# Performance work log

Measured on AMD Instinct MI355X. Metric: run time of the kernel, lower is better.

## Reference

```python
import jax, jax.numpy as jnp
import numpy as np

G, KP, EPS = 4, 9, 1e-5  # deformable groups, 3x3 kernel points, BN eps


def setup_inputs() -> dict:
    key = jax.random.key(0)
    ks = jax.random.split(key, 16)
    N, C1, C2, H, W = 8, 256, 256, 64, 64
    c = int(C1 * 1.0) // 16 * 16  # 256 internal width
    OM = int(np.ceil(G * KP * 3 / 8) * 8)  # 112 padded offset/mask dim (108 used)
    sd = 0.02
    return {
        "x": jax.random.normal(ks[0], (N, C1, H, W), jnp.float32),
        "cv1_w": jax.random.normal(ks[1], (c, C1), jnp.float32) * sd,
        "cv1_b": jax.random.normal(ks[2], (c,), jnp.float32) * sd,
        "value_w": jax.random.normal(ks[3], (c, c), jnp.float32) * sd,
        "value_b": jax.random.normal(ks[4], (c,), jnp.float32) * sd,
        "dw_w": jax.random.normal(ks[5], (c,), jnp.float32) * sd + 1.0,
        "dw_b": jax.random.normal(ks[6], (c,), jnp.float32) * sd,
        "om_w": jax.random.normal(ks[7], (OM, c), jnp.float32) * sd,
        "om_b": jax.random.normal(ks[8], (OM,), jnp.float32) * sd,
        "out_w": jax.random.normal(ks[9], (c, c), jnp.float32) * sd,
        "cv2_w": jax.random.normal(ks[10], (C2, c), jnp.float32) * sd,
        "bn_gamma": jnp.ones((C2,), jnp.float32),
        "bn_beta": jnp.zeros((C2,), jnp.float32),
        "bn_mean": jax.random.normal(ks[11], (C2,), jnp.float32) * 0.1,
        "bn_var": jax.random.uniform(ks[12], (C2,), jnp.float32, minval=0.5, maxval=1.5),
    }


def _dcnv4(value, offset_mask, H, W):
    """DCNv4 core: offset-based bilinear sampling + unnormalized-mask aggregation.
    value: (N,H,W,c) NHWC features; offset_mask: (N,H,W,OM), per group layout
    [2*KP offsets (dx,dy pairs), KP masks]; no softmax on masks (DCNv4)."""
    N, c = value.shape[0], value.shape[-1]
    GC = c // G
    om = offset_mask[..., : G * KP * 3].reshape(N, H, W, G, 3 * KP)
    offs = om[..., : 2 * KP].reshape(N, H, W, G, KP, 2)  # (dx, dy), x = width axis
    mask = om[..., 2 * KP:]                               # (N,H,W,G,KP)
    ky, kx = jnp.meshgrid(jnp.arange(-1, 2, dtype=jnp.float32),
                          jnp.arange(-1, 2, dtype=jnp.float32), indexing="ij")
    kx, ky = kx.reshape(KP), ky.reshape(KP)               # 3x3 dilation-1 grid
    base_x = jnp.arange(W, dtype=jnp.float32)[None, None, :, None, None]
    base_y = jnp.arange(H, dtype=jnp.float32)[None, :, None, None, None]
    px = base_x + kx + offs[..., 0]                       # (N,H,W,G,KP) abs pixel x
    py = base_y + ky + offs[..., 1]
    x0, y0 = jnp.floor(px), jnp.floor(py)
    fx, fy = px - x0, py - y0
    x0i, y0i = x0.astype(jnp.int32), y0.astype(jnp.int32)
    vflat = value.reshape(N, H * W, G, GC).transpose(0, 2, 1, 3)  # (N,G,L,GC)
    acc = jnp.zeros((N, G, H, W, KP, GC), value.dtype)
    for dy, dx, wgt in ((0, 0, (1 - fy) * (1 - fx)), (0, 1, (1 - fy) * fx),
                        (1, 0, fy * (1 - fx)), (1, 1, fy * fx)):
        yy, xx = y0i + dy, x0i + dx
        valid = (yy >= 0) & (yy < H) & (xx >= 0) & (xx < W)   # zero padding
        idx = jnp.clip(yy, 0, H - 1) * W + jnp.clip(xx, 0, W - 1)
        idx_g = idx.transpose(0, 3, 1, 2, 4).reshape(N, G, H * W * KP)
        smp = jnp.take_along_axis(vflat, idx_g[..., None], axis=2)
        smp = smp.reshape(N, G, H, W, KP, GC)
        acc = acc + smp * (wgt * valid).transpose(0, 3, 1, 2, 4)[..., None]
    out = (acc * mask.transpose(0, 3, 1, 2, 4)[..., None]).sum(axis=4)  # (N,G,H,W,GC)
    return out.transpose(0, 2, 3, 1, 4).reshape(N, H, W, c)


def reference(x, cv1_w, cv1_b, value_w, value_b, dw_w, dw_b, om_w, om_b,
              out_w, cv2_w, bn_gamma, bn_beta, bn_mean, bn_var):
    N, C1, H, W = x.shape
    t = jnp.einsum("nchw,dc->nhwd", x, cv1_w) + cv1_b       # cv1 1x1 conv -> NHWC
    value = t @ value_w.T + value_b                          # DCNv4 value_proj
    om = (t * dw_w + dw_b) @ om_w.T + om_b                   # depthwise 1x1 + linear
    y = _dcnv4(value, om, H, W)
    y = y @ out_w.T                                          # output_proj (no bias)
    y = jnp.einsum("nhwc,dc->nhwd", y, cv2_w)                # cv2 1x1 (no bias)
    y = (y - bn_mean) * bn_gamma * jax.lax.rsqrt(bn_var + EPS) + bn_beta  # BN (eval)
    y = y * jax.nn.sigmoid(y)                                # SiLU
    return y.transpose(0, 3, 1, 2)                           # back to NCHW
```

## Files before the change

### kernel.cpp

```cpp
#include <hip/hip_runtime.h>
#include <hip/hip_bf16.h>
#include <math.h>

#define NN    8
#define HH    64
#define WW    64
#define HW    4096
#define NHW   32768
#define DALL  384
#define EPSBN 1e-5f

typedef __attribute__((ext_vector_type(8))) short short8v;
typedef __attribute__((ext_vector_type(4))) float f32x4;

__device__ __forceinline__ float b2f(unsigned short u) {
    union { unsigned int i; float f; } v; v.i = ((unsigned int)u) << 16; return v.f;
}
__device__ __forceinline__ unsigned short f2b(float f) {
    __hip_bfloat16 h = __float2bfloat16(f);
    return *reinterpret_cast<const unsigned short*>(&h);
}


__global__ __launch_bounds__(256)
void prep_kernel(const float* __restrict__ cv1_w, const float* __restrict__ cv1_b,
                 const float* __restrict__ value_w, const float* __restrict__ value_b,
                 const float* __restrict__ dw_w, const float* __restrict__ dw_b,
                 const float* __restrict__ om_w, const float* __restrict__ om_b,
                 const float* __restrict__ out_w, const float* __restrict__ cv2_w,
                 const float* __restrict__ bn_g, const float* __restrict__ bn_b,
                 const float* __restrict__ bn_m, const float* __restrict__ bn_v,
                 unsigned short* __restrict__ Wallbf, float* __restrict__ ball,
                 unsigned short* __restrict__ Woutbf, float* __restrict__ bout)
{
    int job = blockIdx.x * 256 + threadIdx.x;
    if (job < 65536) {
        int d = job >> 8, cc = job & 255;
        float s = 0.f;
        for (int e = 0; e < 256; ++e)
            s = fmaf(value_w[d*256+e], cv1_w[e*256+cc], s);
        Wallbf[job] = f2b(s);
    } else if (job < 94208) {
        int idx = job - 65536;
        int o = idx >> 8, cc = idx & 255;
        float s = 0.f;
        for (int e = 0; e < 256; ++e)
            s = fmaf(om_w[o*256+e]*dw_w[e], cv1_w[e*256+cc], s);
        Wallbf[job] = f2b(s);
    } else if (job < 98304) {
        Wallbf[job] = 0;
    } else if (job < 163840) {
        int idx = job - 98304;
        int d = idx >> 8;
        float s = 0.f;
        for (int e = 0; e < 256; ++e)
            s = fmaf(cv2_w[d*256+e], out_w[e*256 + (idx & 255)], s);
        float sc = bn_g[d] * rsqrtf(bn_v[d] + EPSBN);
        Woutbf[idx] = f2b(s * sc);
    } else if (job < 164096) {
        int d = job - 163840;
        float s = value_b[d];
        for (int e = 0; e < 256; ++e) s = fmaf(value_w[d*256+e], cv1_b[e], s);
        ball[d] = s;
    } else if (job < 164208) {
        int o = job - 164096;
        float s = om_b[o];
        for (int e = 0; e < 256; ++e)
            s = fmaf(om_w[o*256+e], fmaf(dw_w[e], cv1_b[e], dw_b[e]), s);
        ball[256 + o] = s;
    } else if (job < 164224) {
        ball[368 + job - 164208] = 0.f;
    } else if (job < 164480) {
        int d = job - 164224;
        float sc = bn_g[d] * rsqrtf(bn_v[d] + EPSBN);
        bout[d] = fmaf(-bn_m[d], sc, bn_b[d]);
    }
}

__global__ __launch_bounds__(256)
void cvt_tr_kernel(const float* __restrict__ x, unsigned short* __restrict__ xt)
{
    __shared__ float Ls[64][65];
    int p0 = blockIdx.x * 64;
    int c0 = blockIdx.y * 64;
    int n = p0 >> 12, hw0 = p0 & 4095;
    int t = threadIdx.x;
    #pragma unroll
    for (int i = 0; i < 16; ++i) {
        int idx = t + i * 256;
        int cc = idx >> 6, pp = idx & 63;
        Ls[cc][pp] = x[((size_t)(n*256 + c0 + cc))*4096 + hw0 + pp];
    }
    __syncthreads();
    #pragma unroll
    for (int i = 0; i < 8; ++i) {
        int idx = t + i * 256;
        int pp = idx >> 5, cp = idx & 31;
        int c = cp * 2;
        ushort2 v;
        v.x = f2b(Ls[c][pp]);
        v.y = f2b(Ls[c+1][pp]);
        *reinterpret_cast<ushort2*>(&xt[(size_t)(p0 + pp)*256 + c0 + c]) = v;
    }
}

__device__ __forceinline__
void gemm_mainloop(const unsigned short* __restrict__ A, const unsigned short* __restrict__ B,
                   int m0, int n0, unsigned short* As, unsigned short* Bs,
                   f32x4 (&acc)[4][4], int t)
{
    int lane = t & 63;
    int wv = t >> 6;
    int wr = wv >> 1, wc = wv & 1;
    int r_l = lane & 15;
    int kg_l = lane >> 4;

    for (int kt = 0; kt < 4; ++kt) {
        int c0 = kt * 64;
        #pragma unroll
        for (int i = 0; i < 4; ++i) {
            int idx = t + i * 256;
            int kg = idx & 7, row = idx >> 3;
            int soff = row*64 + ((kg ^ (row & 7)) << 3);
            *reinterpret_cast<short8v*>(&As[soff]) =
                *reinterpret_cast<const short8v*>(&A[(size_t)(m0 + row)*256 + c0 + kg*8]);
            *reinterpret_cast<short8v*>(&Bs[soff]) =
                *reinterpret_cast<const short8v*>(&B[(size_t)(n0 + row)*256 + c0 + kg*8]);
        }
        __syncthreads();
        #pragma unroll
        for (int ks = 0; ks < 2; ++ks) {
            short8v af[4], bfr[4];
            #pragma unroll
            for (int m = 0; m < 4; ++m) {
                int row = wr*64 + m*16 + r_l;
                af[m] = *reinterpret_cast<const short8v*>(
                    &As[row*64 + (((ks*4 + kg_l) ^ (row & 7)) << 3)]);
            }
            #pragma unroll
            for (int n = 0; n < 4; ++n) {
                int row = wc*64 + n*16 + r_l;
                bfr[n] = *reinterpret_cast<const short8v*>(
                    &Bs[row*64 + (((ks*4 + kg_l) ^ (row & 7)) << 3)]);
            }
            #pragma unroll
            for (int m = 0; m < 4; ++m)
                #pragma unroll
                for (int n = 0; n < 4; ++n)
                    acc[m][n] = __builtin_amdgcn_mfma_f32_16x16x32_bf16(af[m], bfr[n], acc[m][n], 0, 0, 0);
        }
        __syncthreads();
    }
}

__global__ __launch_bounds__(256)
void gemm_vo_kernel(const unsigned short* __restrict__ xt, const unsigned short* __restrict__ Wallbf,
                    const float* __restrict__ ball, unsigned short* __restrict__ VO)
{
    __shared__ unsigned short lds[2 * 8192];
    int t = threadIdx.x;
    int m0 = blockIdx.x * 128;
    int n0 = blockIdx.y * 128;
    f32x4 acc[4][4] = {};
    gemm_mainloop(xt, Wallbf, m0, n0, lds, lds + 8192, acc, t);

    int lane = t & 63;
    int wv = t >> 6, wr = wv >> 1, wc = wv & 1;
    int r_l = lane & 15, kg_l = lane >> 4;
    #pragma unroll
    for (int n = 0; n < 4; ++n) {
        int d = n0 + wc*64 + n*16 + r_l;
        float bb = ball[d];
        #pragma unroll
        for (int m = 0; m < 4; ++m) {
            int pr = m0 + wr*64 + m*16 + (kg_l << 2);
            #pragma unroll
            for (int r = 0; r < 4; ++r)
                VO[(size_t)(pr + r)*384 + d] = f2b(acc[m][n][r] + bb);
        }
    }
}

__global__ __launch_bounds__(256)
void gemm_out_kernel(const unsigned short* __restrict__ Woutbf, const unsigned short* __restrict__ y,
                     const float* __restrict__ bout, float* __restrict__ out)
{
    __shared__ unsigned short lds[2 * 8192];
    int t = threadIdx.x;
    int m0 = blockIdx.y * 128;
    int n0 = blockIdx.x * 128;
    f32x4 acc[4][4] = {};
    gemm_mainloop(Woutbf, y, m0, n0, lds, lds + 8192, acc, t);

    int lane = t & 63;
    int wv = t >> 6, wr = wv >> 1, wc = wv & 1;
    int r_l = lane & 15, kg_l = lane >> 4;
    int nimg = n0 >> 12;
    int hwb = n0 & 4095;
    #pragma unroll
    for (int m = 0; m < 4; ++m) {
        int dbase = m0 + wr*64 + m*16 + (kg_l << 2);
        #pragma unroll
        for (int r = 0; r < 4; ++r) {
            int d = dbase + r;
            float bb = bout[d];
            #pragma unroll
            for (int n = 0; n < 4; ++n) {
                int pcol = wc*64 + n*16 + r_l;
                float z = acc[m][n][r] + bb;
                float sv = z / (1.f + __expf(-z));
                out[((size_t)(nimg*256 + d))*4096 + hwb + pcol] = sv;
            }
        }
    }
}

__global__ __launch_bounds__(256)
void dcn_kernel(const unsigned short* __restrict__ VO, unsigned short* __restrict__ y)
{
    __shared__ float om_s[8][108];
    int t = threadIdx.x;
    int p0 = blockIdx.x * 8;

    for (int i = t; i < 864; i += 256) {
        int pl = i / 108, j = i - pl * 108;
        om_s[pl][j] = b2f(VO[(size_t)(p0 + pl)*384 + 256 + j]);
    }
    __syncthreads();

    int slot = t >> 3, ch8 = t & 7;
    int pl = slot >> 2, g = slot & 3;
    int p = p0 + pl;
    int hw = p & 4095;
    int h = hw >> 6, w = hw & 63;
    const unsigned short* vbase = VO + (size_t)(p >> 12) * (HW * (size_t)DALL) + g*64 + ch8*8;
    const float* o = &om_s[pl][g*27];

    float acc[8] = {};
    #pragma unroll
    for (int k = 0; k < 9; ++k) {
        float dxo = o[2*k], dyo = o[2*k+1], m = o[18+k];
        float pxf = (float)(w + (k % 3) - 1) + dxo;
        float pyf = (float)(h + (k / 3) - 1) + dyo;
        float x0f = floorf(pxf), y0f = floorf(pyf);
        float fx = pxf - x0f, fy = pyf - y0f;
        int x0 = (int)x0f, y0 = (int)y0f;
        #pragma unroll
        for (int dyy = 0; dyy < 2; ++dyy) {
            #pragma unroll
            for (int dxx = 0; dxx < 2; ++dxx) {
                int yy = y0 + dyy, xx = x0 + dxx;
                bool valid = (yy >= 0) & (yy < HH) & (xx >= 0) & (xx < WW);
                float wgt = (dyy ? fy : 1.f - fy) * (dxx ? fx : 1.f - fx);
                float wm = valid ? (m * wgt) : 0.f;
                int yc = min(max(yy, 0), HH - 1);
                int xc = min(max(xx, 0), WW - 1);
                short8v v = *reinterpret_cast<const short8v*>(
                    &vbase[(size_t)(yc * WW + xc) * DALL]);
                #pragma unroll
                for (int c = 0; c < 8; ++c)
                    acc[c] = fmaf(b2f((unsigned short)v[c]), wm, acc[c]);
            }
        }
    }
    short8v ov;
    #pragma unroll
    for (int c = 0; c < 8; ++c) ov[c] = (short)f2b(acc[c]);
    *reinterpret_cast<short8v*>(&y[(size_t)p*256 + g*64 + ch8*8]) = ov;
}

extern "C" void kernel_launch(void* const* d_in, const int* in_sizes, int n_in,
                              void* d_out, int out_size, void* d_ws, size_t ws_size,
                              hipStream_t stream) {
    const float* x       = (const float*)d_in[0];
    const float* cv1_w   = (const float*)d_in[1];
    const float* cv1_b   = (const float*)d_in[2];
    const float* value_w = (const float*)d_in[3];
    const float* value_b = (const float*)d_in[4];
    const float* dw_w    = (const float*)d_in[5];
    const float* dw_b    = (const float*)d_in[6];
    const float* om_w    = (const float*)d_in[7];
    const float* om_b    = (const float*)d_in[8];
    const float* out_w   = (const float*)d_in[9];
    const float* cv2_w   = (const float*)d_in[10];
    const float* bn_g    = (const float*)d_in[11];
    const float* bn_b    = (const float*)d_in[12];
    const float* bn_m    = (const float*)d_in[13];
    const float* bn_v    = (const float*)d_in[14];

    char* ws = (char*)d_ws;
    unsigned short* xt     = (unsigned short*)(ws);
    unsigned short* VO     = (unsigned short*)(ws + 16777216);
    unsigned short* y      = (unsigned short*)(ws + 41943040);
    unsigned short* Wallbf = (unsigned short*)(ws + 58720256);
    unsigned short* Woutbf = (unsigned short*)(ws + 58916864);
    float*          ball   = (float*)(ws + 59047936);
    float*          bout   = (float*)(ws + 59049472);
    float* out = (float*)d_out;

    prep_kernel<<<643, 256, 0, stream>>>(cv1_w, cv1_b, value_w, value_b, dw_w, dw_b,
                                         om_w, om_b, out_w, cv2_w,
                                         bn_g, bn_b, bn_m, bn_v,
                                         Wallbf, ball, Woutbf, bout);
    cvt_tr_kernel<<<dim3(512, 4), 256, 0, stream>>>(x, xt);
    gemm_vo_kernel<<<dim3(256, 3), 256, 0, stream>>>(xt, Wallbf, ball, VO);
    dcn_kernel<<<4096, 256, 0, stream>>>(VO, y);
    gemm_out_kernel<<<dim3(256, 2), 256, 0, stream>>>(Woutbf, y, bout, out);
}
```

Baseline: 95.96 us.

## Fuse NCHW transpose into value GEMM, tile DCN sampling via LDS, vectorize prep

Removes the separate fp32-to-bf16 transpose kernel: the value/offset GEMM now reads NCHW fp32 input directly, converts it in registers, and writes swizzled tiles into LDS. The DCN kernel now stages a 5x20 neighbourhood of value rows per 16-pixel chunk in shared memory and falls back to global loads only for out-of-tile samples. It also uses packed float2 FMAs. Prep loops get float4 loads with four independent accumulators. The costs are a larger LDS footprint, more blocks re-reading the 3x3 halo (each value tile is loaded by two group-half blocks), and a strided fp32 read pattern in the GEMM load.

```diff
diff --git a/kernel.cpp b/kernel.cpp
--- a/kernel.cpp
+++ b/kernel.cpp
@@ -12,6 +12,7 @@
 
 typedef __attribute__((ext_vector_type(8))) short short8v;
 typedef __attribute__((ext_vector_type(4))) float f32x4;
+typedef __attribute__((ext_vector_type(2))) float f32x2;
 
 __device__ __forceinline__ float b2f(unsigned short u) {
     union { unsigned int i; float f; } v; v.i = ((unsigned int)u) << 16; return v.f;
@@ -19,6 +20,12 @@
 __device__ __forceinline__ unsigned short f2b(float f) {
     __hip_bfloat16 h = __float2bfloat16(f);
     return *reinterpret_cast<const unsigned short*>(&h);
+}
+__device__ __forceinline__ f32x2 bf2x(int u) {
+    union { int i; float f; } a, b;
+    a.i = u << 16;
+    b.i = u & 0xffff0000;
+    f32x2 r; r[0] = a.f; r[1] = b.f; return r;
 }
 
 
@@ -36,27 +43,43 @@
     int job = blockIdx.x * 256 + threadIdx.x;
     if (job < 65536) {
         int d = job >> 8, cc = job & 255;
-        float s = 0.f;
-        for (int e = 0; e < 256; ++e)
-            s = fmaf(value_w[d*256+e], cv1_w[e*256+cc], s);
-        Wallbf[job] = f2b(s);
+        float s0=0.f, s1=0.f, s2=0.f, s3=0.f;
+        for (int e = 0; e < 256; e += 4) {
+            float4 wv = *reinterpret_cast<const float4*>(&value_w[d*256+e]);
+            s0 = fmaf(wv.x, cv1_w[(e+0)*256+cc], s0);
+            s1 = fmaf(wv.y, cv1_w[(e+1)*256+cc], s1);
+            s2 = fmaf(wv.z, cv1_w[(e+2)*256+cc], s2);
+            s3 = fmaf(wv.w, cv1_w[(e+3)*256+cc], s3);
+        }
+        Wallbf[job] = f2b((s0+s1)+(s2+s3));
     } else if (job < 94208) {
         int idx = job - 65536;
         int o = idx >> 8, cc = idx & 255;
-        float s = 0.f;
-        for (int e = 0; e < 256; ++e)
-            s = fmaf(om_w[o*256+e]*dw_w[e], cv1_w[e*256+cc], s);
-        Wallbf[job] = f2b(s);
+        float s0=0.f, s1=0.f, s2=0.f, s3=0.f;
+        for (int e = 0; e < 256; e += 4) {
+            float4 wv = *reinterpret_cast<const float4*>(&om_w[o*256+e]);
+            float4 dv = *reinterpret_cast<const float4*>(&dw_w[e]);
+            s0 = fmaf(wv.x*dv.x, cv1_w[(e+0)*256+cc], s0);
+            s1 = fmaf(wv.y*dv.y, cv1_w[(e+1)*256+cc], s1);
+            s2 = fmaf(wv.z*dv.z, cv1_w[(e+2)*256+cc], s2);
+            s3 = fmaf(wv.w*dv.w, cv1_w[(e+3)*256+cc], s3);
+        }
+        Wallbf[job] = f2b((s0+s1)+(s2+s3));
     } else if (job < 98304) {
         Wallbf[job] = 0;
     } else if (job < 163840) {
         int idx = job - 98304;
-        int d = idx >> 8;
-        float s = 0.f;
-        for (int e = 0; e < 256; ++e)
-            s = fmaf(cv2_w[d*256+e], out_w[e*256 + (idx & 255)], s);
+        int d = idx >> 8, cc = idx & 255;
+        float s0=0.f, s1=0.f, s2=0.f, s3=0.f;
+        for (int e = 0; e < 256; e += 4) {
+            float4 wv = *reinterpret_cast<const float4*>(&cv2_w[d*256+e]);
+            s0 = fmaf(wv.x, out_w[(e+0)*256+cc], s0);
+            s1 = fmaf(wv.y, out_w[(e+1)*256+cc], s1);
+            s2 = fmaf(wv.z, out_w[(e+2)*256+cc], s2);
+            s3 = fmaf(wv.w, out_w[(e+3)*256+cc], s3);
+        }
         float sc = bn_g[d] * rsqrtf(bn_v[d] + EPSBN);
-        Woutbf[idx] = f2b(s * sc);
+        Woutbf[idx] = f2b(((s0+s1)+(s2+s3)) * sc);
     } else if (job < 164096) {
         int d = job - 163840;
         float s = value_b[d];
@@ -78,29 +101,89 @@
 }
 
 __global__ __launch_bounds__(256)
-void cvt_tr_kernel(const float* __restrict__ x, unsigned short* __restrict__ xt)
+void gemm_vo_kernel(const float* __restrict__ x, const unsigned short* __restrict__ Wallbf,
+                    const float* __restrict__ ball, unsigned short* __restrict__ VO)
 {
-    __shared__ float Ls[64][65];
-    int p0 = blockIdx.x * 64;
-    int c0 = blockIdx.y * 64;
-    int n = p0 >> 12, hw0 = p0 & 4095;
+    __shared__ unsigned short As[8192];
+    __shared__ unsigned short Bs[8192];
     int t = threadIdx.x;
-    #pragma unroll
-    for (int i = 0; i < 16; ++i) {
-        int idx = t + i * 256;
-        int cc = idx >> 6, pp = idx & 63;
-        Ls[cc][pp] = x[((size_t)(n*256 + c0 + cc))*4096 + hw0 + pp];
-    }
-    __syncthreads();
-    #pragma unroll
-    for (int i = 0; i < 8; ++i) {
-        int idx = t + i * 256;
-        int pp = idx >> 5, cp = idx & 31;
-        int c = cp * 2;
-        ushort2 v;
-        v.x = f2b(Ls[c][pp]);
-        v.y = f2b(Ls[c+1][pp]);
-        *reinterpret_cast<ushort2*>(&xt[(size_t)(p0 + pp)*256 + c0 + c]) = v;
+    int m0 = blockIdx.x * 128;
+    int n0 = blockIdx.y * 128;
+    int nimg = m0 >> 12, hw0 = m0 & 4095;
+    int lane = t & 63;
+    int wv = t >> 6;
+    int wr = wv >> 1, wc = wv & 1;
+    int r_l = lane & 15, kg_l = lane >> 4;
+    int ci = t >> 6;
+    int l  = t & 63;
+
+    const float* xbase = x + (size_t)(nimg * 256) * 4096 + hw0;
+
+    f32x4 acc[4][4] = {};
+
+    for (int kt = 0; kt < 4; ++kt) {
+        int c0 = kt * 64;
+        float2 val[16];
+        #pragma unroll
+        for (int i = 0; i < 16; ++i)
+            val[i] = *reinterpret_cast<const float2*>(
+                &xbase[(size_t)(c0 + ci*16 + i) * 4096 + 2*l]);
+        __syncthreads();
+        #pragma unroll
+        for (int rsel = 0; rsel < 2; ++rsel) {
+            int row = 2*l + rsel;
+            #pragma unroll
+            for (int kgi = 0; kgi < 2; ++kgi) {
+                int kg = ci*2 + kgi;
+                short8v s;
+                #pragma unroll
+                for (int j = 0; j < 8; ++j)
+                    s[j] = (short)f2b(rsel ? val[kgi*8+j].y : val[kgi*8+j].x);
+                *reinterpret_cast<short8v*>(&As[row*64 + ((kg ^ (row & 7)) << 3)]) = s;
+            }
+        }
+        #pragma unroll
+        for (int i = 0; i < 4; ++i) {
+            int idx = t + i*256;
+            int row = idx >> 3, kg = idx & 7;
+            *reinterpret_cast<short8v*>(&Bs[row*64 + ((kg ^ (row & 7)) << 3)]) =
+                *reinterpret_cast<const short8v*>(&Wallbf[(size_t)(n0 + row)*256 + c0 + kg*8]);
+        }
+        __syncthreads();
+        #pragma unroll
+        for (int ks = 0; ks < 2; ++ks) {
+            short8v af[4], bfr[4];
+            #pragma unroll
+            for (int m = 0; m < 4; ++m) {
+                int row = wr*64 + m*16 + r_l;
+                af[m] = *reinterpret_cast<const short8v*>(
+                    &As[row*64 + (((ks*4 + kg_l) ^ (row & 7)) << 3)]);
+            }
+            #pragma unroll
+            for (int n = 0; n < 4; ++n) {
+                int row = wc*64 + n*16 + r_l;
+                bfr[n] = *reinterpret_cast<const short8v*>(
+                    &Bs[row*64 + (((ks*4 + kg_l) ^ (row & 7)) << 3)]);
+            }
+            #pragma unroll
+            for (int m = 0; m < 4; ++m)
+                #pragma unroll
+                for (int n = 0; n < 4; ++n)
+                    acc[m][n] = __builtin_amdgcn_mfma_f32_16x16x32_bf16(af[m], bfr[n], acc[m][n], 0, 0, 0);
+        }
+    }
+
+    #pragma unroll
+    for (int n = 0; n < 4; ++n) {
+        int d = n0 + wc*64 + n*16 + r_l;
+        float bb = ball[d];
+        #pragma unroll
+        for (int m = 0; m < 4; ++m) {
+            int pr = m0 + wr*64 + m*16 + (kg_l << 2);
+            #pragma unroll
+            for (int r = 0; r < 4; ++r)
+                VO[(size_t)(pr + r)*384 + d] = f2b(acc[m][n][r] + bb);
+        }
     }
 }
 
@@ -154,34 +237,6 @@
 }
 
 __global__ __launch_bounds__(256)
-void gemm_vo_kernel(const unsigned short* __restrict__ xt, const unsigned short* __restrict__ Wallbf,
-                    const float* __restrict__ ball, unsigned short* __restrict__ VO)
-{
-    __shared__ unsigned short lds[2 * 8192];
-    int t = threadIdx.x;
-    int m0 = blockIdx.x * 128;
-    int n0 = blockIdx.y * 128;
-    f32x4 acc[4][4] = {};
-    gemm_mainloop(xt, Wallbf, m0, n0, lds, lds + 8192, acc, t);
-
-    int lane = t & 63;
-    int wv = t >> 6, wr = wv >> 1, wc = wv & 1;
-    int r_l = lane & 15, kg_l = lane >> 4;
-    #pragma unroll
-    for (int n = 0; n < 4; ++n) {
-        int d = n0 + wc*64 + n*16 + r_l;
-        float bb = ball[d];
-        #pragma unroll
-        for (int m = 0; m < 4; ++m) {
-            int pr = m0 + wr*64 + m*16 + (kg_l << 2);
-            #pragma unroll
-            for (int r = 0; r < 4; ++r)
-                VO[(size_t)(pr + r)*384 + d] = f2b(acc[m][n][r] + bb);
-        }
-    }
-}
-
-__global__ __launch_bounds__(256)
 void gemm_out_kernel(const unsigned short* __restrict__ Woutbf, const unsigned short* __restrict__ y,
                      const float* __restrict__ bout, float* __restrict__ out)
 {
@@ -218,25 +273,51 @@
 __global__ __launch_bounds__(256)
 void dcn_kernel(const unsigned short* __restrict__ VO, unsigned short* __restrict__ y)
 {
-    __shared__ float om_s[8][108];
+    __shared__ unsigned short vt[5*20*128];
+    __shared__ float om_s[16][54];
+    int bid = blockIdx.x;
+    int chunk = bid >> 1, gs = bid & 1;
+    int p0 = chunk * 16;
+    int n = p0 >> 12;
+    int hw0 = p0 & 4095;
+    int h = hw0 >> 6, w0 = hw0 & 63;
     int t = threadIdx.x;
-    int p0 = blockIdx.x * 8;
-
-    for (int i = t; i < 864; i += 256) {
-        int pl = i / 108, j = i - pl * 108;
-        om_s[pl][j] = b2f(VO[(size_t)(p0 + pl)*384 + 256 + j]);
+
+    const unsigned short* vimg = VO + (size_t)n * (HW * (size_t)DALL);
+
+    #pragma unroll
+    for (int j = 0; j < 7; ++j) {
+        int s = t + j*256;
+        if (s < 1600) {
+            int ch8 = s & 15;
+            int cr = s >> 4;
+            int col = cr % 20;
+            int row = cr / 20;
+            int vr = min(max(h - 2 + row, 0), 63);
+            int vc = min(max(w0 - 2 + col, 0), 63);
+            *reinterpret_cast<short8v*>(&vt[(row*20 + col)*128 + ch8*8]) =
+                *reinterpret_cast<const short8v*>(
+                    &vimg[(size_t)(vr*64 + vc)*DALL + gs*128 + ch8*8]);
+        }
+    }
+    #pragma unroll
+    for (int j = 0; j < 4; ++j) {
+        int s = t + j*256;
+        if (s < 864) {
+            int pxl = s / 54;
+            int r = s - pxl*54;
+            om_s[pxl][r] = b2f(vimg[(size_t)(hw0 + pxl)*DALL + 256 + gs*54 + r]);
+        }
     }
     __syncthreads();
 
     int slot = t >> 3, ch8 = t & 7;
-    int pl = slot >> 2, g = slot & 3;
-    int p = p0 + pl;
-    int hw = p & 4095;
-    int h = hw >> 6, w = hw & 63;
-    const unsigned short* vbase = VO + (size_t)(p >> 12) * (HW * (size_t)DALL) + g*64 + ch8*8;
-    const float* o = &om_s[pl][g*27];
-
-    float acc[8] = {};
+    int pxl = slot >> 1, gl = slot & 1;
+    int w = w0 + pxl;
+    const float* o = om_s[pxl] + gl*27;
+    const unsigned short* vgbase = vimg + gs*128 + gl*64 + ch8*8;
+
+    f32x2 acc2[4] = {};
     #pragma unroll
     for (int k = 0; k < 9; ++k) {
         float dxo = o[2*k], dyo = o[2*k+1], m = o[18+k];
@@ -252,21 +333,35 @@
                 int yy = y0 + dyy, xx = x0 + dxx;
                 bool valid = (yy >= 0) & (yy < HH) & (xx >= 0) & (xx < WW);
                 float wgt = (dyy ? fy : 1.f - fy) * (dxx ? fx : 1.f - fx);
-                float wm = valid ? (m * wgt) : 0.f;
-                int yc = min(max(yy, 0), HH - 1);
-                int xc = min(max(xx, 0), WW - 1);
-                short8v v = *reinterpret_cast<const short8v*>(
-                    &vbase[(size_t)(yc * WW + xc) * DALL]);
+                float wmc = valid ? (m * wgt) : 0.f;
+                int ry = yy - (h - 2), rx = xx - (w0 - 2);
+                bool intile = ((unsigned)ry < 5u) & ((unsigned)rx < 20u);
+                int4 v;
+                if (intile | (wmc == 0.f)) {
+                    int ryc = min(max(ry, 0), 4), rxc = min(max(rx, 0), 19);
+                    v = *reinterpret_cast<const int4*>(&vt[(ryc*20 + rxc)*128 + gl*64 + ch8*8]);
+                } else {
+                    int yc = min(max(yy, 0), HH - 1);
+                    int xc = min(max(xx, 0), WW - 1);
+                    v = *reinterpret_cast<const int4*>(&vgbase[(size_t)(yc*64 + xc)*DALL]);
+                }
+                f32x2 wm2; wm2[0] = wmc; wm2[1] = wmc;
+                int vv[4] = {v.x, v.y, v.z, v.w};
                 #pragma unroll
-                for (int c = 0; c < 8; ++c)
-                    acc[c] = fmaf(b2f((unsigned short)v[c]), wm, acc[c]);
+                for (int q = 0; q < 4; ++q) {
+                    f32x2 val2 = bf2x(vv[q]);
+                    acc2[q] += val2 * wm2;
+                }
             }
         }
     }
     short8v ov;
     #pragma unroll
-    for (int c = 0; c < 8; ++c) ov[c] = (short)f2b(acc[c]);
-    *reinterpret_cast<short8v*>(&y[(size_t)p*256 + g*64 + ch8*8]) = ov;
+    for (int q = 0; q < 4; ++q) {
+        ov[2*q]   = (short)f2b(acc2[q][0]);
+        ov[2*q+1] = (short)f2b(acc2[q][1]);
+    }
+    *reinterpret_cast<short8v*>(&y[(size_t)(p0+pxl)*256 + (gs*2+gl)*64 + ch8*8]) = ov;
 }
 
 extern "C" void kernel_launch(void* const* d_in, const int* in_sizes, int n_in,
@@ -289,21 +384,19 @@
     const float* bn_v    = (const float*)d_in[14];
 
     char* ws = (char*)d_ws;
-    unsigned short* xt     = (unsigned short*)(ws);
-    unsigned short* VO     = (unsigned short*)(ws + 16777216);
-    unsigned short* y      = (unsigned short*)(ws + 41943040);
-    unsigned short* Wallbf = (unsigned short*)(ws + 58720256);
-    unsigned short* Woutbf = (unsigned short*)(ws + 58916864);
-    float*          ball   = (float*)(ws + 59047936);
-    float*          bout   = (float*)(ws + 59049472);
+    unsigned short* VO     = (unsigned short*)(ws);
+    unsigned short* y      = (unsigned short*)(ws + 25165824);
+    unsigned short* Wallbf = (unsigned short*)(ws + 41943040);
+    unsigned short* Woutbf = (unsigned short*)(ws + 42139648);
+    float*          ball   = (float*)(ws + 42270720);
+    float*          bout   = (float*)(ws + 42272256);
     float* out = (float*)d_out;
 
     prep_kernel<<<643, 256, 0, stream>>>(cv1_w, cv1_b, value_w, value_b, dw_w, dw_b,
                                          om_w, om_b, out_w, cv2_w,
                                          bn_g, bn_b, bn_m, bn_v,
                                          Wallbf, ball, Woutbf, bout);
-    cvt_tr_kernel<<<dim3(512, 4), 256, 0, stream>>>(x, xt);
-    gemm_vo_kernel<<<dim3(256, 3), 256, 0, stream>>>(xt, Wallbf, ball, VO);
+    gemm_vo_kernel<<<dim3(256, 3), 256, 0, stream>>>(x, Wallbf, ball, VO);
     dcn_kernel<<<4096, 256, 0, stream>>>(VO, y);
     gemm_out_kernel<<<dim3(256, 2), 256, 0, stream>>>(Woutbf, y, bout, out);
 }
```

Result: slower. 124.0 us (+29.2%).
